# Optimization experiments

Measured on AMD Instinct MI355X. Metric: run time of the kernel, lower is better.

## Reference

```python
import jax, jax.numpy as jnp
import numpy as np

N = 100000
E = 1600000
D = 128      # input feature dim
H = 128      # hidden_channels
O = 2        # out_channels
NEG_SLOPE = 0.2
EPS = 1e-16  # PyG softmax denominator epsilon


def gat_conv(x, src, dst, W_src, W_dst, att_src, att_dst, bias):
    """PyG GATConv, heads=1, add_self_loops=False, concat=True."""
    xs = x @ W_src                      # [N, C]
    xd = x @ W_dst                      # [N, C]
    a_s = xs @ att_src                  # [N]
    a_d = xd @ att_dst                  # [N]
    e = jax.nn.leaky_relu(a_s[src] + a_d[dst], NEG_SLOPE)   # [E]
    # segment softmax over edges grouped by destination node
    m = jax.ops.segment_max(e, dst, num_segments=N)          # [N]
    m = jnp.where(jnp.isfinite(m), m, 0.0)
    ex = jnp.exp(e - m[dst])                                  # [E]
    denom = jax.ops.segment_sum(ex, dst, num_segments=N)      # [N]
    alpha = ex / (denom[dst] + EPS)                            # [E]
    msg = alpha[:, None] * xs[src]                             # [E, C]
    out = jax.ops.segment_sum(msg, dst, num_segments=N)       # [N, C]
    return out + bias


def setup_inputs() -> dict:
    key = jax.random.key(0)
    ks = jax.random.split(key, 14)
    s = lambda k, shape, fan: jax.random.normal(k, shape, jnp.float32) * (1.0 / np.sqrt(fan))
    x = jax.random.normal(ks[0], (N, D), jnp.float32)
    edge_index = jax.random.randint(ks[1], (2, E), 0, N, dtype=jnp.int32)
    return {
        "x": x,
        "edge_index": edge_index,
        "W1s": s(ks[2], (D, H), D), "W1d": s(ks[3], (D, H), D),
        "a1s": s(ks[4], (H,), H),   "a1d": s(ks[5], (H,), H),
        "b1": jnp.zeros((H,), jnp.float32),
        "W2s": s(ks[6], (H, H), H), "W2d": s(ks[7], (H, H), H),
        "a2s": s(ks[8], (H,), H),   "a2d": s(ks[9], (H,), H),
        "b2": jnp.zeros((H,), jnp.float32),
        "Wl": s(ks[10], (H, O), H), "bl": jnp.zeros((O,), jnp.float32),
    }


def reference(x, edge_index, W1s, W1d, a1s, a1d, b1, W2s, W2d, a2s, a2d, b2, Wl, bl):
    src, dst = edge_index[0], edge_index[1]
    h = jax.nn.relu(gat_conv(x, src, dst, W1s, W1d, a1s, a1d, b1))
    # dropout p=0.3 is identity at inference
    h = jax.nn.relu(gat_conv(h, src, dst, W2s, W2d, a2s, a2d, b2))
    return h @ Wl + bl  # [N, O]
```

## Files before the change

### kernel.cpp

```cpp
#include <hip/hip_runtime.h>
#include <hip/hip_fp16.h>

#define NBSHIFT 8
#define BSZ     256
#define CAP     5120

typedef _Float16 f16x8 __attribute__((ext_vector_type(8)));
typedef float    f32x4 __attribute__((ext_vector_type(4)));


#define GEMM_LDS_BYTES (128 * 136 * 2 + 512)

template <bool XHALF>
__device__ __forceinline__ void gemm_body(
        const void* __restrict__ Xv, const float* __restrict__ Ws,
        const float* __restrict__ Wd, const float* __restrict__ attd,
        const float* __restrict__ att,
        __half* __restrict__ Y, float* __restrict__ a_s, float* __restrict__ a_d,
        int N, int blk, char* smem) {
    _Float16 (*sWh)[136] = (_Float16(*)[136])smem;
    float* svd = (float*)(smem + 128 * 136 * 2);
    int t = threadIdx.x;

    if (t < 128) {
        const float4* wr = (const float4*)&Wd[t * 128];
        const float4* ar = (const float4*)attd;
        float s = 0.f;
#pragma unroll 8
        for (int j = 0; j < 32; j++) {
            float4 w = wr[j], a = ar[j];
            s += w.x * a.x + w.y * a.y + w.z * a.z + w.w * a.w;
        }
        svd[t] = s;
    }
#pragma unroll
    for (int i = 0; i < 16; i++) {
        int gid = t + i * 256;
        int n = gid & 127, kq = gid >> 7;
        _Float16 p[4];
        p[0] = (_Float16)Ws[(kq * 4 + 0) * 128 + n];
        p[1] = (_Float16)Ws[(kq * 4 + 1) * 128 + n];
        p[2] = (_Float16)Ws[(kq * 4 + 2) * 128 + n];
        p[3] = (_Float16)Ws[(kq * 4 + 3) * 128 + n];
        *(uint2*)&sWh[n][kq * 4] = *(uint2*)p;
    }
    __syncthreads();

    int l = t & 63, wv = t >> 6;
    int quad = l >> 4, lm = l & 15;
    int rbase = blk * 64 + wv * 16;
    int arow = rbase + lm;
    bool rok = arow < N;

    f32x4 acc[8];
#pragma unroll
    for (int c = 0; c < 8; c++) acc[c] = (f32x4){0.f, 0.f, 0.f, 0.f};
    float adp = 0.f;

#pragma unroll
    for (int kc = 0; kc < 4; kc++) {
        int k0 = kc * 32 + quad * 8;
        float xf[8];
        f16x8 af;
        if constexpr (XHALF) {
            const __half* xrow = (const __half*)Xv + (size_t)arow * 128;
            if (rok) {
                af = *(const f16x8*)&xrow[k0];
            } else {
#pragma unroll
                for (int j = 0; j < 8; j++) af[j] = (_Float16)0.f;
            }
#pragma unroll
            for (int j = 0; j < 8; j++) xf[j] = (float)af[j];
        } else {
            const float* xrow = (const float*)Xv + (size_t)arow * 128;
            if (rok) {
                *(float4*)&xf[0] = *(const float4*)&xrow[k0];
                *(float4*)&xf[4] = *(const float4*)&xrow[k0 + 4];
            } else {
#pragma unroll
                for (int j = 0; j < 8; j++) xf[j] = 0.f;
            }
#pragma unroll
            for (int j = 0; j < 8; j++) af[j] = (_Float16)xf[j];
        }
        float4 v0 = *(const float4*)&svd[k0];
        float4 v1 = *(const float4*)&svd[k0 + 4];
        adp += xf[0] * v0.x + xf[1] * v0.y + xf[2] * v0.z + xf[3] * v0.w
             + xf[4] * v1.x + xf[5] * v1.y + xf[6] * v1.z + xf[7] * v1.w;
#pragma unroll
        for (int c = 0; c < 8; c++) {
            f16x8 bf = *(const f16x8*)&sWh[c * 16 + lm][k0];
            acc[c] = __builtin_amdgcn_mfma_f32_16x16x32_f16(af, bf, acc[c], 0, 0, 0);
        }
    }

    adp += __shfl_xor(adp, 16);
    adp += __shfl_xor(adp, 32);
    if (quad == 0 && rok) a_d[arow] = adp;

    float attc[8];
#pragma unroll
    for (int c = 0; c < 8; c++) attc[c] = att[c * 16 + lm];
#pragma unroll
    for (int r = 0; r < 4; r++) {
        int grow = rbase + quad * 4 + r;
        bool gok = grow < N;
        float p = 0.f;
#pragma unroll
        for (int c = 0; c < 8; c++) {
            if (gok) Y[(size_t)grow * 128 + c * 16 + lm] = __float2half(acc[c][r]);
            p += acc[c][r] * attc[c];
        }
        p += __shfl_xor(p, 1); p += __shfl_xor(p, 2); p += __shfl_xor(p, 4); p += __shfl_xor(p, 8);
        if (lm == 0 && gok) a_s[grow] = p;
    }
}

__global__ __launch_bounds__(256, 4) void k_fuse1(
        const float* __restrict__ X, const float* __restrict__ W1s,
        const float* __restrict__ W1d, const float* __restrict__ a1d,
        const float* __restrict__ a1s,
        __half* __restrict__ Y, float* __restrict__ a_s, float* __restrict__ a_d, int N, int gb,
        const int* __restrict__ src, const int* __restrict__ dst, int E,
        int* __restrict__ cursor, unsigned* __restrict__ pairs) {
    __shared__ __align__(16) char smem[GEMM_LDS_BYTES];
    int t = threadIdx.x;

    if ((int)blockIdx.x >= gb) {
        int* hist  = (int*)smem;
        int* start = hist + 512;
        hist[t] = 0; hist[t + 256] = 0;
        __syncthreads();
        int e0 = (blockIdx.x - gb) * 1024 + t * 4;
        int d[4], s[4];
        bool full = (e0 + 3 < E);
        if (full) {
            int4 dv = *(const int4*)&dst[e0];
            int4 sv = *(const int4*)&src[e0];
            d[0] = dv.x; d[1] = dv.y; d[2] = dv.z; d[3] = dv.w;
            s[0] = sv.x; s[1] = sv.y; s[2] = sv.z; s[3] = sv.w;
#pragma unroll
            for (int i = 0; i < 4; i++) atomicAdd(&hist[d[i] >> NBSHIFT], 1);
        } else {
#pragma unroll
            for (int i = 0; i < 4; i++) {
                if (e0 + i < E) { d[i] = dst[e0 + i]; s[i] = src[e0 + i]; atomicAdd(&hist[d[i] >> NBSHIFT], 1); }
                else d[i] = -1;
            }
        }
        __syncthreads();
        if (hist[t] > 0)       start[t]       = atomicAdd(&cursor[t],       hist[t]);
        if (hist[t + 256] > 0) start[t + 256] = atomicAdd(&cursor[t + 256], hist[t + 256]);
        __syncthreads();
        hist[t] = 0; hist[t + 256] = 0;
        __syncthreads();
#pragma unroll
        for (int i = 0; i < 4; i++) {
            if (full || (e0 + i < E)) {
                int b = d[i] >> NBSHIFT;
                int r = atomicAdd(&hist[b], 1);
                pairs[b * CAP + start[b] + r] = ((unsigned)(d[i] & (BSZ - 1)) << 17) | (unsigned)s[i];
            }
        }
        return;
    }

    gemm_body<false>(X, W1s, W1d, a1d, a1s, Y, a_s, a_d, N, blockIdx.x, smem);
}

__global__ __launch_bounds__(256, 4) void k_gemm2(
        const __half* __restrict__ X, const float* __restrict__ W2s,
        const float* __restrict__ W2d, const float* __restrict__ a2d,
        const float* __restrict__ a2s,
        __half* __restrict__ Y, float* __restrict__ a_s, float* __restrict__ a_d, int N) {
    __shared__ __align__(16) char smem[GEMM_LDS_BYTES];
    gemm_body<true>(X, W2s, W2d, a2d, a2s, Y, a_s, a_d, N, blockIdx.x, smem);
}

__global__ __launch_bounds__(256) void kB_csr(const unsigned* __restrict__ pairs,
                                              const int* __restrict__ cursor,
                                              int* __restrict__ row_start, int* __restrict__ row_end,
                                              int* __restrict__ csr_src, int N) {
    __shared__ int cnt[BSZ];
    __shared__ int cur[BSZ];
    __shared__ int sS[256];
    int b = blockIdx.x, t = threadIdx.x;
    int base = b * CAP;
    int ecnt = cursor[b];
    int nodeBase = b << NBSHIFT;
    cnt[t] = 0;
    __syncthreads();
    for (int j = t; j < ecnt; j += 256)
        atomicAdd(&cnt[pairs[base + j] >> 17], 1);
    __syncthreads();
    int c0 = cnt[t];
    sS[t] = c0; __syncthreads();
    for (int off = 1; off < 256; off <<= 1) {
        int x = (t >= off) ? sS[t - off] : 0;
        __syncthreads();
        sS[t] += x;
        __syncthreads();
    }
    int excl = sS[t] - c0;
    cur[t] = excl;
    int g = nodeBase + t;
    if (g < N) { row_start[g] = base + excl; row_end[g] = base + excl + c0; }
    __syncthreads();
    for (int j = t; j < ecnt; j += 256) {
        unsigned p = pairs[base + j];
        int r = atomicAdd(&cur[p >> 17], 1);
        csr_src[base + r] = (int)(p & 0x1FFFFu);
    }
}


__device__ __forceinline__ void fma_mix2(float& a0, float& a1, unsigned h2, float w) {
    asm("v_fma_mix_f32 %0, %1, %2, %0 op_sel_hi:[1,0,0]" : "+v"(a0) : "v"(h2), "v"(w));
    asm("v_fma_mix_f32 %0, %1, %2, %0 op_sel:[1,0,0] op_sel_hi:[1,0,0]" : "+v"(a1) : "v"(h2), "v"(w));
}

#define ACC_MIX(u, wj)  do {                                    \
    const unsigned* _w32 = (const unsigned*)&(u);               \
    fma_mix2(acc[0], acc[1], _w32[0], (wj));                    \
    fma_mix2(acc[2], acc[3], _w32[1], (wj));                    \
    fma_mix2(acc[4], acc[5], _w32[2], (wj));                    \
    fma_mix2(acc[6], acc[7], _w32[3], (wj));                    \
} while (0)

template <bool HEAD>
__global__ __launch_bounds__(256, 6) void k_agg(const int* __restrict__ csr_src, const int* __restrict__ rs_,
                                                const int* __restrict__ re_,
                                                const float* __restrict__ a_s, const float* __restrict__ a_d,
                                                const __half* __restrict__ xs, const float* __restrict__ bias,
                                                const float* __restrict__ Wl, const float* __restrict__ bl,
                                                void* __restrict__ outv, int N) {
    __shared__ int2 sP[4][4][16];
    int t = threadIdx.x; int wv = t >> 6, l = t & 63;
    int q = l >> 4, es = l & 15;
    int n = blockIdx.x * 16 + wv * 4 + q;
    bool nok = n < N;
    int rs0 = 0, deg = 0;
    if (nok) { rs0 = rs_[n]; deg = re_[n] - rs0; }
    float adn = nok ? a_d[n] : 0.f;
    const int* cs = csr_src + rs0;
    int c = es * 8;

    int R = (deg + 15) >> 4;
    R = max(R, __shfl_xor(R, 16));
    R = max(R, __shfl_xor(R, 32));

    float acc[8];
#pragma unroll
    for (int k = 0; k < 8; k++) acc[k] = 0.f;
    float dnl = 0.f;
    int2 (*sq)[16] = sP[wv];

    for (int r = 0; r < R; ++r) {
        int i = r * 16 + es;
        int idx = 0; float w = 0.f;
        if (i < deg) {
            idx = cs[i];
            float tv = a_s[idx] + adn;
            tv = tv > 0.f ? tv : 0.2f * tv;
            w = __expf(tv);
        }
        dnl += w;
        sq[q][es] = make_int2(idx, __float_as_int(w));

        int rem = deg - r * 16;
        int mcq = rem >= 16 ? 16 : (rem > 0 ? ((rem + 3) & ~3) : 0);
        const int2* spq = sq[q];
        for (int e = 0; e < mcq; e += 4) {
            int4 pA = *(const int4*)&spq[e];
            int4 pB = *(const int4*)&spq[e + 2];
            uint4 u0 = *(const uint4*)&xs[(size_t)pA.x * 128 + c];
            uint4 u1 = *(const uint4*)&xs[(size_t)pA.z * 128 + c];
            uint4 u2 = *(const uint4*)&xs[(size_t)pB.x * 128 + c];
            uint4 u3 = *(const uint4*)&xs[(size_t)pB.z * 128 + c];
            ACC_MIX(u0, __int_as_float(pA.y));
            ACC_MIX(u1, __int_as_float(pA.w));
            ACC_MIX(u2, __int_as_float(pB.y));
            ACC_MIX(u3, __int_as_float(pB.w));
        }
    }

    dnl += __shfl_xor(dnl, 1);
    dnl += __shfl_xor(dnl, 2);
    dnl += __shfl_xor(dnl, 4);
    dnl += __shfl_xor(dnl, 8);
    float inv = 1.f / (dnl + 1e-16f);

    float hv[8];
    float4 b0 = *(const float4*)&bias[c];
    float4 b1 = *(const float4*)&bias[c + 4];
    float bb[8] = {b0.x, b0.y, b0.z, b0.w, b1.x, b1.y, b1.z, b1.w};
#pragma unroll
    for (int k = 0; k < 8; k++) {
        float v = acc[k] * inv + bb[k];
        hv[k] = v > 0.f ? v : 0.f;
    }

    if (HEAD) {
        float p0 = 0.f, p1 = 0.f;
#pragma unroll
        for (int k = 0; k < 8; k++) {
            p0 += hv[k] * Wl[2 * (c + k)];
            p1 += hv[k] * Wl[2 * (c + k) + 1];
        }
        p0 += __shfl_xor(p0, 1); p0 += __shfl_xor(p0, 2);
        p0 += __shfl_xor(p0, 4); p0 += __shfl_xor(p0, 8);
        p1 += __shfl_xor(p1, 1); p1 += __shfl_xor(p1, 2);
        p1 += __shfl_xor(p1, 4); p1 += __shfl_xor(p1, 8);
        if (es == 0 && nok) {
            float* out = (float*)outv;
            out[2 * n]     = p0 + bl[0];
            out[2 * n + 1] = p1 + bl[1];
        }
    } else {
        if (nok) {
            __half* hout = (__half*)outv;
            __half hb[8];
#pragma unroll
            for (int k = 0; k < 8; k++) hb[k] = __float2half(hv[k]);
            *(uint4*)&hout[(size_t)n * 128 + c] = *(uint4*)hb;
        }
    }
}


extern "C" void kernel_launch(void* const* d_in, const int* in_sizes, int n_in,
                              void* d_out, int out_size, void* d_ws, size_t ws_size,
                              hipStream_t stream) {
    const float* x   = (const float*)d_in[0];
    const int*   ei  = (const int*)d_in[1];
    const float* W1s = (const float*)d_in[2];
    const float* W1d = (const float*)d_in[3];
    const float* a1s = (const float*)d_in[4];
    const float* a1d = (const float*)d_in[5];
    const float* b1  = (const float*)d_in[6];
    const float* W2s = (const float*)d_in[7];
    const float* W2d = (const float*)d_in[8];
    const float* a2s = (const float*)d_in[9];
    const float* a2d = (const float*)d_in[10];
    const float* b2  = (const float*)d_in[11];
    const float* Wl  = (const float*)d_in[12];
    const float* bl  = (const float*)d_in[13];
    float* out = (float*)d_out;

    int N = in_sizes[0] / 128;
    int E = in_sizes[1] / 2;
    const int* srcA = ei;
    const int* dstA = ei + E;
    int NB = (N + BSZ - 1) >> NBSHIFT;

    __half* xs = (__half*)d_ws;
    __half* h  = xs + (size_t)N * 128;
    float* as_ = (float*)(h + (size_t)N * 128);
    float* ad_ = as_ + N;
    int* row_start = (int*)(ad_ + N);
    int* row_end   = row_start + N;
    int* csr_src   = row_end + N;
    int* cursor    = csr_src + (size_t)NB * CAP;
    unsigned* pairs = (unsigned*)h;

    int gb = (N + 63) / 64;
    int EB = (E + 1023) / 1024;
    int ab = (N + 15) / 16;

    hipMemsetAsync(cursor, 0, (size_t)NB * 4, stream);

    k_fuse1<<<gb + EB, 256, 0, stream>>>(x, W1s, W1d, a1d, a1s, xs, as_, ad_, N, gb,
                                         srcA, dstA, E, cursor, pairs);

    kB_csr<<<NB, 256, 0, stream>>>(pairs, cursor, row_start, row_end, csr_src, N);

    k_agg<false><<<ab, 256, 0, stream>>>(csr_src, row_start, row_end, as_, ad_, xs, b1, nullptr, nullptr, h, N);

    k_gemm2<<<gb, 256, 0, stream>>>(h, W2s, W2d, a2d, a2s, xs, as_, ad_, N);

    k_agg<true><<<ab, 256, 0, stream>>>(csr_src, row_start, row_end, as_, ad_, xs, b2, Wl, bl, out, N);
}
```

Before: 319.7 us.

## Build CSR via degree histogram and scan; loop GEMM blocks over rows

Drops the two-pass bucketed pair sort (block histograms plus a per-bucket CSR kernel) and builds the CSR with a per-node degree histogram kernel, a per-bucket prefix scan, and a direct scatter of source ids using global atomics on per-node cursors. The scatter stays fused into the first GEMM launch. The GEMM blocks now each handle four 64-row groups, so the fp16 weight staging into LDS is amortised over more rows. The cost is one extra launch, many more global atomics contending on node counters, and fewer GEMM blocks. Edge order within a row also becomes nondeterministic.

After: 587.2 us. 1.84x slower.

```diff
diff --git a/kernel.cpp b/kernel.cpp
--- a/kernel.cpp
+++ b/kernel.cpp
@@ -4,6 +4,7 @@
 #define NBSHIFT 8
 #define BSZ     256
 #define CAP     5120
+#define ROWG    4
 
 typedef _Float16 f16x8 __attribute__((ext_vector_type(8)));
 typedef float    f32x4 __attribute__((ext_vector_type(4)));
@@ -48,73 +49,114 @@
 
     int l = t & 63, wv = t >> 6;
     int quad = l >> 4, lm = l & 15;
-    int rbase = blk * 64 + wv * 16;
-    int arow = rbase + lm;
-    bool rok = arow < N;
-
-    f32x4 acc[8];
-#pragma unroll
-    for (int c = 0; c < 8; c++) acc[c] = (f32x4){0.f, 0.f, 0.f, 0.f};
-    float adp = 0.f;
-
-#pragma unroll
-    for (int kc = 0; kc < 4; kc++) {
-        int k0 = kc * 32 + quad * 8;
-        float xf[8];
-        f16x8 af;
-        if constexpr (XHALF) {
-            const __half* xrow = (const __half*)Xv + (size_t)arow * 128;
-            if (rok) {
-                af = *(const f16x8*)&xrow[k0];
+
+    float attc[8];
+#pragma unroll
+    for (int c = 0; c < 8; c++) attc[c] = att[c * 16 + lm];
+
+    for (int g = 0; g < ROWG; ++g) {
+        int rbase = blk * (64 * ROWG) + g * 64 + wv * 16;
+        int arow = rbase + lm;
+        bool rok = arow < N;
+
+        f32x4 acc[8];
+#pragma unroll
+        for (int c = 0; c < 8; c++) acc[c] = (f32x4){0.f, 0.f, 0.f, 0.f};
+        float adp = 0.f;
+
+#pragma unroll
+        for (int kc = 0; kc < 4; kc++) {
+            int k0 = kc * 32 + quad * 8;
+            float xf[8];
+            f16x8 af;
+            if constexpr (XHALF) {
+                const __half* xrow = (const __half*)Xv + (size_t)arow * 128;
+                if (rok) {
+                    af = *(const f16x8*)&xrow[k0];
+                } else {
+#pragma unroll
+                    for (int j = 0; j < 8; j++) af[j] = (_Float16)0.f;
+                }
+#pragma unroll
+                for (int j = 0; j < 8; j++) xf[j] = (float)af[j];
             } else {
-#pragma unroll
-                for (int j = 0; j < 8; j++) af[j] = (_Float16)0.f;
+                const float* xrow = (const float*)Xv + (size_t)arow * 128;
+                if (rok) {
+                    *(float4*)&xf[0] = *(const float4*)&xrow[k0];
+                    *(float4*)&xf[4] = *(const float4*)&xrow[k0 + 4];
+                } else {
+#pragma unroll
+                    for (int j = 0; j < 8; j++) xf[j] = 0.f;
+                }
+#pragma unroll
+                for (int j = 0; j < 8; j++) af[j] = (_Float16)xf[j];
             }
-#pragma unroll
-            for (int j = 0; j < 8; j++) xf[j] = (float)af[j];
+            float4 v0 = *(const float4*)&svd[k0];
+            float4 v1 = *(const float4*)&svd[k0 + 4];
+            adp += xf[0] * v0.x + xf[1] * v0.y + xf[2] * v0.z + xf[3] * v0.w
+                 + xf[4] * v1.x + xf[5] * v1.y + xf[6] * v1.z + xf[7] * v1.w;
+#pragma unroll
+            for (int c = 0; c < 8; c++) {
+                f16x8 bf = *(const f16x8*)&sWh[c * 16 + lm][k0];
+                acc[c] = __builtin_amdgcn_mfma_f32_16x16x32_f16(af, bf, acc[c], 0, 0, 0);
+            }
+        }
+
+        adp += __shfl_xor(adp, 16);
+        adp += __shfl_xor(adp, 32);
+        if (quad == 0 && rok) a_d[arow] = adp;
+
+#pragma unroll
+        for (int r = 0; r < 4; r++) {
+            int grow = rbase + quad * 4 + r;
+            bool gok = grow < N;
+            float p = 0.f;
+#pragma unroll
+            for (int c = 0; c < 8; c++) {
+                if (gok) Y[(size_t)grow * 128 + c * 16 + lm] = __float2half(acc[c][r]);
+                p += acc[c][r] * attc[c];
+            }
+            p += __shfl_xor(p, 1); p += __shfl_xor(p, 2); p += __shfl_xor(p, 4); p += __shfl_xor(p, 8);
+            if (lm == 0 && gok) a_s[grow] = p;
+        }
+    }
+}
+
+__global__ __launch_bounds__(256) void kH(const int* __restrict__ dst, int* __restrict__ deg, int E) {
+    int t = threadIdx.x;
+#pragma unroll
+    for (int j = 0; j < 4; j++) {
+        int e = blockIdx.x * 4096 + j * 1024 + t * 4;
+        if (e + 3 < E) {
+            int4 d = *(const int4*)&dst[e];
+            atomicAdd(&deg[d.x], 1);
+            atomicAdd(&deg[d.y], 1);
+            atomicAdd(&deg[d.z], 1);
+            atomicAdd(&deg[d.w], 1);
         } else {
-            const float* xrow = (const float*)Xv + (size_t)arow * 128;
-            if (rok) {
-                *(float4*)&xf[0] = *(const float4*)&xrow[k0];
-                *(float4*)&xf[4] = *(const float4*)&xrow[k0 + 4];
-            } else {
-#pragma unroll
-                for (int j = 0; j < 8; j++) xf[j] = 0.f;
-            }
-#pragma unroll
-            for (int j = 0; j < 8; j++) af[j] = (_Float16)xf[j];
-        }
-        float4 v0 = *(const float4*)&svd[k0];
-        float4 v1 = *(const float4*)&svd[k0 + 4];
-        adp += xf[0] * v0.x + xf[1] * v0.y + xf[2] * v0.z + xf[3] * v0.w
-             + xf[4] * v1.x + xf[5] * v1.y + xf[6] * v1.z + xf[7] * v1.w;
-#pragma unroll
-        for (int c = 0; c < 8; c++) {
-            f16x8 bf = *(const f16x8*)&sWh[c * 16 + lm][k0];
-            acc[c] = __builtin_amdgcn_mfma_f32_16x16x32_f16(af, bf, acc[c], 0, 0, 0);
-        }
-    }
-
-    adp += __shfl_xor(adp, 16);
-    adp += __shfl_xor(adp, 32);
-    if (quad == 0 && rok) a_d[arow] = adp;
-
-    float attc[8];
-#pragma unroll
-    for (int c = 0; c < 8; c++) attc[c] = att[c * 16 + lm];
-#pragma unroll
-    for (int r = 0; r < 4; r++) {
-        int grow = rbase + quad * 4 + r;
-        bool gok = grow < N;
-        float p = 0.f;
-#pragma unroll
-        for (int c = 0; c < 8; c++) {
-            if (gok) Y[(size_t)grow * 128 + c * 16 + lm] = __float2half(acc[c][r]);
-            p += acc[c][r] * attc[c];
-        }
-        p += __shfl_xor(p, 1); p += __shfl_xor(p, 2); p += __shfl_xor(p, 4); p += __shfl_xor(p, 8);
-        if (lm == 0 && gok) a_s[grow] = p;
-    }
+            for (int i = 0; i < 4; i++)
+                if (e + i < E) atomicAdd(&deg[dst[e + i]], 1);
+        }
+    }
+}
+
+__global__ __launch_bounds__(256) void k_scan(int* __restrict__ deg,
+                                              int* __restrict__ row_start, int* __restrict__ row_end,
+                                              int N) {
+    __shared__ int sS[256];
+    int b = blockIdx.x, t = threadIdx.x;
+    int g = b * 256 + t;
+    int d = (g < N) ? deg[g] : 0;
+    sS[t] = d; __syncthreads();
+    for (int off = 1; off < 256; off <<= 1) {
+        int x = (t >= off) ? sS[t - off] : 0;
+        __syncthreads();
+        sS[t] += x;
+        __syncthreads();
+    }
+    int excl = sS[t] - d;
+    int base = b * CAP + excl;
+    if (g < N) { row_start[g] = base; row_end[g] = base + d; deg[g] = base; }
 }
 
 __global__ __launch_bounds__(256, 4) void k_fuse1(
@@ -123,44 +165,29 @@
         const float* __restrict__ a1s,
         __half* __restrict__ Y, float* __restrict__ a_s, float* __restrict__ a_d, int N, int gb,
         const int* __restrict__ src, const int* __restrict__ dst, int E,
-        int* __restrict__ cursor, unsigned* __restrict__ pairs) {
+        int* __restrict__ cur, int* __restrict__ csr_src) {
     __shared__ __align__(16) char smem[GEMM_LDS_BYTES];
     int t = threadIdx.x;
 
     if ((int)blockIdx.x >= gb) {
-        int* hist  = (int*)smem;
-        int* start = hist + 512;
-        hist[t] = 0; hist[t + 256] = 0;
-        __syncthreads();
-        int e0 = (blockIdx.x - gb) * 1024 + t * 4;
-        int d[4], s[4];
-        bool full = (e0 + 3 < E);
-        if (full) {
-            int4 dv = *(const int4*)&dst[e0];
-            int4 sv = *(const int4*)&src[e0];
-            d[0] = dv.x; d[1] = dv.y; d[2] = dv.z; d[3] = dv.w;
-            s[0] = sv.x; s[1] = sv.y; s[2] = sv.z; s[3] = sv.w;
-#pragma unroll
-            for (int i = 0; i < 4; i++) atomicAdd(&hist[d[i] >> NBSHIFT], 1);
-        } else {
-#pragma unroll
-            for (int i = 0; i < 4; i++) {
-                if (e0 + i < E) { d[i] = dst[e0 + i]; s[i] = src[e0 + i]; atomicAdd(&hist[d[i] >> NBSHIFT], 1); }
-                else d[i] = -1;
-            }
-        }
-        __syncthreads();
-        if (hist[t] > 0)       start[t]       = atomicAdd(&cursor[t],       hist[t]);
-        if (hist[t + 256] > 0) start[t + 256] = atomicAdd(&cursor[t + 256], hist[t + 256]);
-        __syncthreads();
-        hist[t] = 0; hist[t + 256] = 0;
-        __syncthreads();
-#pragma unroll
-        for (int i = 0; i < 4; i++) {
-            if (full || (e0 + i < E)) {
-                int b = d[i] >> NBSHIFT;
-                int r = atomicAdd(&hist[b], 1);
-                pairs[b * CAP + start[b] + r] = ((unsigned)(d[i] & (BSZ - 1)) << 17) | (unsigned)s[i];
+        int base = ((int)blockIdx.x - gb) * 4096;
+#pragma unroll
+        for (int j = 0; j < 4; j++) {
+            int e = base + j * 1024 + t * 4;
+            if (e + 3 < E) {
+                int4 dv = *(const int4*)&dst[e];
+                int4 sv = *(const int4*)&src[e];
+                int r0 = atomicAdd(&cur[dv.x], 1); csr_src[r0] = sv.x;
+                int r1 = atomicAdd(&cur[dv.y], 1); csr_src[r1] = sv.y;
+                int r2 = atomicAdd(&cur[dv.z], 1); csr_src[r2] = sv.z;
+                int r3 = atomicAdd(&cur[dv.w], 1); csr_src[r3] = sv.w;
+            } else {
+                for (int i = 0; i < 4; i++) {
+                    if (e + i < E) {
+                        int r = atomicAdd(&cur[dst[e + i]], 1);
+                        csr_src[r] = src[e + i];
+                    }
+                }
             }
         }
         return;
@@ -176,42 +203,6 @@
         __half* __restrict__ Y, float* __restrict__ a_s, float* __restrict__ a_d, int N) {
     __shared__ __align__(16) char smem[GEMM_LDS_BYTES];
     gemm_body<true>(X, W2s, W2d, a2d, a2s, Y, a_s, a_d, N, blockIdx.x, smem);
-}
-
-__global__ __launch_bounds__(256) void kB_csr(const unsigned* __restrict__ pairs,
-                                              const int* __restrict__ cursor,
-                                              int* __restrict__ row_start, int* __restrict__ row_end,
-                                              int* __restrict__ csr_src, int N) {
-    __shared__ int cnt[BSZ];
-    __shared__ int cur[BSZ];
-    __shared__ int sS[256];
-    int b = blockIdx.x, t = threadIdx.x;
-    int base = b * CAP;
-    int ecnt = cursor[b];
-    int nodeBase = b << NBSHIFT;
-    cnt[t] = 0;
-    __syncthreads();
-    for (int j = t; j < ecnt; j += 256)
-        atomicAdd(&cnt[pairs[base + j] >> 17], 1);
-    __syncthreads();
-    int c0 = cnt[t];
-    sS[t] = c0; __syncthreads();
-    for (int off = 1; off < 256; off <<= 1) {
-        int x = (t >= off) ? sS[t - off] : 0;
-        __syncthreads();
-        sS[t] += x;
-        __syncthreads();
-    }
-    int excl = sS[t] - c0;
-    cur[t] = excl;
-    int g = nodeBase + t;
-    if (g < N) { row_start[g] = base + excl; row_end[g] = base + excl + c0; }
-    __syncthreads();
-    for (int j = t; j < ecnt; j += 256) {
-        unsigned p = pairs[base + j];
-        int r = atomicAdd(&cur[p >> 17], 1);
-        csr_src[base + r] = (int)(p & 0x1FFFFu);
-    }
 }
 
 
@@ -361,19 +352,20 @@
     int* row_start = (int*)(ad_ + N);
     int* row_end   = row_start + N;
     int* csr_src   = row_end + N;
-    int* cursor    = csr_src + (size_t)NB * CAP;
-    unsigned* pairs = (unsigned*)h;
-
-    int gb = (N + 63) / 64;
-    int EB = (E + 1023) / 1024;
+    int* deg       = csr_src + (size_t)NB * CAP;
+
+    int gb = (N + 64 * ROWG - 1) / (64 * ROWG);
+    int EB = (E + 4095) / 4096;
     int ab = (N + 15) / 16;
 
-    hipMemsetAsync(cursor, 0, (size_t)NB * 4, stream);
+    hipMemsetAsync(deg, 0, (size_t)N * 4, stream);
+
+    kH<<<EB, 256, 0, stream>>>(dstA, deg, E);
+
+    k_scan<<<NB, 256, 0, stream>>>(deg, row_start, row_end, N);
 
     k_fuse1<<<gb + EB, 256, 0, stream>>>(x, W1s, W1d, a1d, a1s, xs, as_, ad_, N, gb,
-                                         srcA, dstA, E, cursor, pairs);
-
-    kB_csr<<<NB, 256, 0, stream>>>(pairs, cursor, row_start, row_end, csr_src, N);
+                                         srcA, dstA, E, deg, csr_src);
 
     k_agg<false><<<ab, 256, 0, stream>>>(csr_src, row_start, row_end, as_, ad_, xs, b1, nullptr, nullptr, h, N);
 
```
